# Kernel tuning notes

Measured on AMD Instinct MI355X. Metric: run time of the kernel, lower is better.

The kernel has to match this reference:

```python
import jax, jax.numpy as jnp
import numpy as np

N, M, D = 8192, 8192, 128
EPS = 1e-9


def setup_inputs() -> dict:
    key = jax.random.key(0)
    k1, k2 = jax.random.split(key)
    X = jax.random.normal(k1, (N, D), dtype=jnp.float32)
    Y = jax.random.normal(k2, (M, D), dtype=jnp.float32)
    sigma = jnp.ones((1,), dtype=jnp.float32)  # bandwidth (self.sigma)
    return {"X": X, "Y": Y, "sigma": sigma}


def reference(X, Y, sigma):
    # l2norm: ||x_i - y_j||^2 = ||x_i||^2 - 2 x_i.y_j + ||y_j||^2
    # (original builds full XX/YY Gram matrices just for their diagonals;
    #  same math via row-wise sums of squares)
    x2 = jnp.sum(X * X, axis=1)          # [n]
    y2 = jnp.sum(Y * Y, axis=1)          # [m]
    xy = jnp.matmul(X, Y.T)              # [n, m]
    dnorm2 = x2[:, None] - 2.0 * xy + y2[None, :]
    sigma2_inv = 1.0 / (sigma[0] ** 2 + EPS)
    K_XY = jnp.exp(-sigma2_inv * dnorm2)  # [n, m]
    return K_XY
```

## Files before the change

kernel.cpp:

```cpp
#include <hip/hip_runtime.h>
#include <stdint.h>

#define D_DIM 128
#define NROW 8192
#define MROW 8192
#define TILE 128
#define LDK2 72
#define OUT_LD 8192

typedef __bf16 bf16x8 __attribute__((ext_vector_type(8)));
typedef float f32x4 __attribute__((ext_vector_type(4)));

__device__ __forceinline__ unsigned short f32_to_bf16(float f) {
    uint32_t u = __float_as_uint(f);
    u = (u + 0x7FFFu + ((u >> 16) & 1u)) >> 16;
    return (unsigned short)u;
}

__global__ __launch_bounds__(256) void rbf_norms(const float* __restrict__ X,
                                                 const float* __restrict__ Y,
                                                 float* __restrict__ nrm) {
    const int t = threadIdx.x;
    const int w = t >> 6, lane = t & 63;
    const int rid = blockIdx.x * 4 + w;
    const float* src = (rid < NROW) ? (X + (size_t)rid * D_DIM)
                                    : (Y + (size_t)(rid - NROW) * D_DIM);
    float2 v = *(const float2*)(src + 2 * lane);
    float s = v.x * v.x + v.y * v.y;
    #pragma unroll
    for (int off = 32; off > 0; off >>= 1) s += __shfl_xor(s, off, 64);
    if (lane == 0) nrm[rid] = s;
}

__global__ __launch_bounds__(256, 4) void rbf_main(const float* __restrict__ X,
                                                   const float* __restrict__ Y,
                                                   const float* __restrict__ sigma,
                                                   const float* __restrict__ nrm,
                                                   float* __restrict__ out) {
    __shared__ unsigned short Xs[TILE][LDK2];
    __shared__ unsigned short Ys[TILE][LDK2];
    __shared__ float x2s[TILE];
    __shared__ float y2s[TILE];

    const int t = threadIdx.x;
    const int row0 = blockIdx.y * TILE;
    const int col0 = blockIdx.x * TILE;

    if (t < 128) x2s[t] = nrm[row0 + t];
    else         y2s[t - 128] = nrm[NROW + col0 + (t - 128)];

    const int w = t >> 6, ln = t & 63;
    const int quad = ln >> 4, l16 = ln & 15;
    const int wr = (w >> 1) * 64;
    const int wc = (w & 1) * 64;

    f32x4 acc[4][4] = {};

    #pragma unroll
    for (int p = 0; p < 2; ++p) {
        #pragma unroll
        for (int i = 0; i < 8; ++i) {
            int f = t + 256 * i;
            int r = f >> 4;
            int c = (f & 15) * 4;
            float4 vx = *(const float4*)(X + (size_t)(row0 + r) * D_DIM + p * 64 + c);
            float4 vy = *(const float4*)(Y + (size_t)(col0 + r) * D_DIM + p * 64 + c);
            ushort4 hx = { f32_to_bf16(vx.x), f32_to_bf16(vx.y), f32_to_bf16(vx.z), f32_to_bf16(vx.w) };
            ushort4 hy = { f32_to_bf16(vy.x), f32_to_bf16(vy.y), f32_to_bf16(vy.z), f32_to_bf16(vy.w) };
            *(ushort4*)(&Xs[r][c]) = hx;
            *(ushort4*)(&Ys[r][c]) = hy;
        }
        __syncthreads();

        #pragma unroll
        for (int ks = 0; ks < 2; ++ks) {
            const int k = ks * 32 + quad * 8;
            bf16x8 ax[4], by[4];
            #pragma unroll
            for (int ti = 0; ti < 4; ++ti)
                ax[ti] = *(const bf16x8*)(&Xs[wr + ti * 16 + l16][k]);
            #pragma unroll
            for (int tj = 0; tj < 4; ++tj)
                by[tj] = *(const bf16x8*)(&Ys[wc + tj * 16 + l16][k]);
            #pragma unroll
            for (int ti = 0; ti < 4; ++ti)
                #pragma unroll
                for (int tj = 0; tj < 4; ++tj)
                    acc[ti][tj] = __builtin_amdgcn_mfma_f32_16x16x32_bf16(by[tj], ax[ti], acc[ti][tj], 0, 0, 0);
        }
        if (p == 0) __syncthreads();
    }

    const float s2 = sigma[0] * sigma[0] + 1e-9f;
    const float cexp = -1.4426950408889634f / s2;

    float x2r[4];
    #pragma unroll
    for (int ti = 0; ti < 4; ++ti) x2r[ti] = x2s[wr + ti * 16 + l16];

    #pragma unroll
    for (int tj = 0; tj < 4; ++tj) {
        f32x4 y2v = *(const f32x4*)(&y2s[wc + tj * 16 + quad * 4]);
        size_t gcol = (size_t)(col0 + wc + tj * 16 + quad * 4);
        #pragma unroll
        for (int ti = 0; ti < 4; ++ti) {
            f32x4 v;
            #pragma unroll
            for (int r = 0; r < 4; ++r) {
                float d = x2r[ti] + y2v[r] - 2.0f * acc[ti][tj][r];
                v[r] = __builtin_amdgcn_exp2f(d * cexp);
            }
            size_t grow = (size_t)(row0 + wr + ti * 16 + l16);
            __builtin_nontemporal_store(v, (f32x4*)(out + grow * OUT_LD + gcol));
        }
    }
}

extern "C" void kernel_launch(void* const* d_in, const int* in_sizes, int n_in,
                              void* d_out, int out_size, void* d_ws, size_t ws_size,
                              hipStream_t stream) {
    const float* X = (const float*)d_in[0];
    const float* Y = (const float*)d_in[1];
    const float* sigma = (const float*)d_in[2];
    float* nrm = (float*)d_ws;
    float* out = (float*)d_out;

    rbf_norms<<<(NROW + MROW) / 4, 256, 0, stream>>>(X, Y, nrm);
    rbf_main<<<dim3(MROW / TILE, NROW / TILE), 256, 0, stream>>>(X, Y, sigma, nrm, out);
}
```

Before: 309.2 us.

## Load MFMA operands directly from global memory, removing LDS staging and barriers

Removes the shared-memory tiles and __syncthreads. Each wave now loads its X/Y fragments straight from global memory into registers and converts them to bf16 with native casts. Row norms are read directly from the workspace instead of through LDS. This drops the LDS round trips and the barriers. In exchange, each X/Y element is fetched by two waves instead of once per block, which relies on L1/L2 to absorb the duplicated traffic, and the global loads are less coalesced.

```diff
diff --git a/kernel.cpp b/kernel.cpp
--- a/kernel.cpp
+++ b/kernel.cpp
@@ -5,16 +5,16 @@
 #define NROW 8192
 #define MROW 8192
 #define TILE 128
-#define LDK2 72
 #define OUT_LD 8192
 
 typedef __bf16 bf16x8 __attribute__((ext_vector_type(8)));
 typedef float f32x4 __attribute__((ext_vector_type(4)));
 
-__device__ __forceinline__ unsigned short f32_to_bf16(float f) {
-    uint32_t u = __float_as_uint(f);
-    u = (u + 0x7FFFu + ((u >> 16) & 1u)) >> 16;
-    return (unsigned short)u;
+__device__ __forceinline__ bf16x8 cvt8(float4 u, float4 v) {
+    bf16x8 r;
+    r[0] = (__bf16)u.x; r[1] = (__bf16)u.y; r[2] = (__bf16)u.z; r[3] = (__bf16)u.w;
+    r[4] = (__bf16)v.x; r[5] = (__bf16)v.y; r[6] = (__bf16)v.z; r[7] = (__bf16)v.w;
+    return r;
 }
 
 __global__ __launch_bounds__(256) void rbf_norms(const float* __restrict__ X,
@@ -37,58 +37,34 @@
                                                    const float* __restrict__ sigma,
                                                    const float* __restrict__ nrm,
                                                    float* __restrict__ out) {
-    __shared__ unsigned short Xs[TILE][LDK2];
-    __shared__ unsigned short Ys[TILE][LDK2];
-    __shared__ float x2s[TILE];
-    __shared__ float y2s[TILE];
-
     const int t = threadIdx.x;
-    const int row0 = blockIdx.y * TILE;
-    const int col0 = blockIdx.x * TILE;
-
-    if (t < 128) x2s[t] = nrm[row0 + t];
-    else         y2s[t - 128] = nrm[NROW + col0 + (t - 128)];
-
     const int w = t >> 6, ln = t & 63;
     const int quad = ln >> 4, l16 = ln & 15;
-    const int wr = (w >> 1) * 64;
-    const int wc = (w & 1) * 64;
+    const int rw = blockIdx.y * TILE + (w >> 1) * 64;
+    const int cw = blockIdx.x * TILE + (w & 1) * 64;
+
+    const float* xr = X + (size_t)(rw + l16) * D_DIM + quad * 8;
+    const float* yr = Y + (size_t)(cw + l16) * D_DIM + quad * 8;
 
     f32x4 acc[4][4] = {};
-
     #pragma unroll
-    for (int p = 0; p < 2; ++p) {
+    for (int ks = 0; ks < 4; ++ks) {
+        bf16x8 a[4], b[4];
         #pragma unroll
-        for (int i = 0; i < 8; ++i) {
-            int f = t + 256 * i;
-            int r = f >> 4;
-            int c = (f & 15) * 4;
-            float4 vx = *(const float4*)(X + (size_t)(row0 + r) * D_DIM + p * 64 + c);
-            float4 vy = *(const float4*)(Y + (size_t)(col0 + r) * D_DIM + p * 64 + c);
-            ushort4 hx = { f32_to_bf16(vx.x), f32_to_bf16(vx.y), f32_to_bf16(vx.z), f32_to_bf16(vx.w) };
-            ushort4 hy = { f32_to_bf16(vy.x), f32_to_bf16(vy.y), f32_to_bf16(vy.z), f32_to_bf16(vy.w) };
-            *(ushort4*)(&Xs[r][c]) = hx;
-            *(ushort4*)(&Ys[r][c]) = hy;
+        for (int tj = 0; tj < 4; ++tj) {
+            const float* p = yr + tj * (16 * D_DIM) + ks * 32;
+            a[tj] = cvt8(*(const float4*)p, *(const float4*)(p + 4));
         }
-        __syncthreads();
-
         #pragma unroll
-        for (int ks = 0; ks < 2; ++ks) {
-            const int k = ks * 32 + quad * 8;
-            bf16x8 ax[4], by[4];
-            #pragma unroll
-            for (int ti = 0; ti < 4; ++ti)
-                ax[ti] = *(const bf16x8*)(&Xs[wr + ti * 16 + l16][k]);
+        for (int ti = 0; ti < 4; ++ti) {
+            const float* p = xr + ti * (16 * D_DIM) + ks * 32;
+            b[ti] = cvt8(*(const float4*)p, *(const float4*)(p + 4));
+        }
+        #pragma unroll
+        for (int ti = 0; ti < 4; ++ti)
             #pragma unroll
             for (int tj = 0; tj < 4; ++tj)
-                by[tj] = *(const bf16x8*)(&Ys[wc + tj * 16 + l16][k]);
-            #pragma unroll
-            for (int ti = 0; ti < 4; ++ti)
-                #pragma unroll
-                for (int tj = 0; tj < 4; ++tj)
-                    acc[ti][tj] = __builtin_amdgcn_mfma_f32_16x16x32_bf16(by[tj], ax[ti], acc[ti][tj], 0, 0, 0);
-        }
-        if (p == 0) __syncthreads();
+                acc[ti][tj] = __builtin_amdgcn_mfma_f32_16x16x32_bf16(a[tj], b[ti], acc[ti][tj], 0, 0, 0);
     }
 
     const float s2 = sigma[0] * sigma[0] + 1e-9f;
@@ -96,12 +72,12 @@
 
     float x2r[4];
     #pragma unroll
-    for (int ti = 0; ti < 4; ++ti) x2r[ti] = x2s[wr + ti * 16 + l16];
+    for (int ti = 0; ti < 4; ++ti) x2r[ti] = nrm[rw + ti * 16 + l16];
 
     #pragma unroll
     for (int tj = 0; tj < 4; ++tj) {
-        f32x4 y2v = *(const f32x4*)(&y2s[wc + tj * 16 + quad * 4]);
-        size_t gcol = (size_t)(col0 + wc + tj * 16 + quad * 4);
+        f32x4 y2v = *(const f32x4*)(nrm + NROW + cw + tj * 16 + quad * 4);
+        size_t gcol = (size_t)(cw + tj * 16 + quad * 4);
         #pragma unroll
         for (int ti = 0; ti < 4; ++ti) {
             f32x4 v;
@@ -110,7 +86,7 @@
                 float d = x2r[ti] + y2v[r] - 2.0f * acc[ti][tj][r];
                 v[r] = __builtin_amdgcn_exp2f(d * cexp);
             }
-            size_t grow = (size_t)(row0 + wr + ti * 16 + l16);
+            size_t grow = (size_t)(rw + ti * 16 + l16);
             __builtin_nontemporal_store(v, (f32x4*)(out + grow * OUT_LD + gcol));
         }
     }
```

New measurement: 379.3 us. 22.7% more time.

## Remap blocks per XCD for L2 locality, use native bf16 convert, drop norm LDS

Applied to the files above, without the earlier changes.

Flattens the grid to 1D and remaps block ids so that blocks landing on the same XCD (round-robin by id mod 8) cover a compact 8x8 group of output tiles, which raises L2 reuse of X and Y rows. It also replaces the manual round-to-nearest-even bf16 conversion with native casts, which may lower to hardware convert instructions. Norms are now read straight from global memory in the epilogue instead of being staged in shared memory. The kernel is dominated by writing the 256MB output, so the gains are limited to load traffic and instruction overhead.

```diff
diff --git a/kernel.cpp b/kernel.cpp
--- a/kernel.cpp
+++ b/kernel.cpp
@@ -11,10 +11,11 @@
 typedef __bf16 bf16x8 __attribute__((ext_vector_type(8)));
 typedef float f32x4 __attribute__((ext_vector_type(4)));
 
-__device__ __forceinline__ unsigned short f32_to_bf16(float f) {
-    uint32_t u = __float_as_uint(f);
-    u = (u + 0x7FFFu + ((u >> 16) & 1u)) >> 16;
-    return (unsigned short)u;
+__device__ __forceinline__ ushort4 cvt4(float4 v) {
+    union { __bf16 h[4]; ushort4 u; } r;
+    r.h[0] = (__bf16)v.x; r.h[1] = (__bf16)v.y;
+    r.h[2] = (__bf16)v.z; r.h[3] = (__bf16)v.w;
+    return r.u;
 }
 
 __global__ __launch_bounds__(256) void rbf_norms(const float* __restrict__ X,
@@ -39,16 +40,16 @@
                                                    float* __restrict__ out) {
     __shared__ unsigned short Xs[TILE][LDK2];
     __shared__ unsigned short Ys[TILE][LDK2];
-    __shared__ float x2s[TILE];
-    __shared__ float y2s[TILE];
+
+    const int b = blockIdx.x;
+    const int xcd = b & 7;
+    const int s = b >> 3;
+    const int grp = s >> 6;
+    const int i = s & 63;
+    const int row0 = (xcd * 8 + (i >> 3)) * TILE;
+    const int col0 = (grp * 8 + (i & 7)) * TILE;
 
     const int t = threadIdx.x;
-    const int row0 = blockIdx.y * TILE;
-    const int col0 = blockIdx.x * TILE;
-
-    if (t < 128) x2s[t] = nrm[row0 + t];
-    else         y2s[t - 128] = nrm[NROW + col0 + (t - 128)];
-
     const int w = t >> 6, ln = t & 63;
     const int quad = ln >> 4, l16 = ln & 15;
     const int wr = (w >> 1) * 64;
@@ -59,16 +60,14 @@
     #pragma unroll
     for (int p = 0; p < 2; ++p) {
         #pragma unroll
-        for (int i = 0; i < 8; ++i) {
-            int f = t + 256 * i;
+        for (int it = 0; it < 8; ++it) {
+            int f = t + 256 * it;
             int r = f >> 4;
             int c = (f & 15) * 4;
             float4 vx = *(const float4*)(X + (size_t)(row0 + r) * D_DIM + p * 64 + c);
             float4 vy = *(const float4*)(Y + (size_t)(col0 + r) * D_DIM + p * 64 + c);
-            ushort4 hx = { f32_to_bf16(vx.x), f32_to_bf16(vx.y), f32_to_bf16(vx.z), f32_to_bf16(vx.w) };
-            ushort4 hy = { f32_to_bf16(vy.x), f32_to_bf16(vy.y), f32_to_bf16(vy.z), f32_to_bf16(vy.w) };
-            *(ushort4*)(&Xs[r][c]) = hx;
-            *(ushort4*)(&Ys[r][c]) = hy;
+            *(ushort4*)(&Xs[r][c]) = cvt4(vx);
+            *(ushort4*)(&Ys[r][c]) = cvt4(vy);
         }
         __syncthreads();
 
@@ -94,23 +93,20 @@
     const float s2 = sigma[0] * sigma[0] + 1e-9f;
     const float cexp = -1.4426950408889634f / s2;
 
-    float x2r[4];
     #pragma unroll
-    for (int ti = 0; ti < 4; ++ti) x2r[ti] = x2s[wr + ti * 16 + l16];
-
-    #pragma unroll
-    for (int tj = 0; tj < 4; ++tj) {
-        f32x4 y2v = *(const f32x4*)(&y2s[wc + tj * 16 + quad * 4]);
-        size_t gcol = (size_t)(col0 + wc + tj * 16 + quad * 4);
+    for (int ti = 0; ti < 4; ++ti) {
+        const float x2 = nrm[row0 + wr + ti * 16 + l16];
+        const size_t grow = (size_t)(row0 + wr + ti * 16 + l16);
         #pragma unroll
-        for (int ti = 0; ti < 4; ++ti) {
+        for (int tj = 0; tj < 4; ++tj) {
+            f32x4 y2v = *(const f32x4*)(nrm + NROW + col0 + wc + tj * 16 + quad * 4);
             f32x4 v;
             #pragma unroll
             for (int r = 0; r < 4; ++r) {
-                float d = x2r[ti] + y2v[r] - 2.0f * acc[ti][tj][r];
+                float d = x2 + y2v[r] - 2.0f * acc[ti][tj][r];
                 v[r] = __builtin_amdgcn_exp2f(d * cexp);
             }
-            size_t grow = (size_t)(row0 + wr + ti * 16 + l16);
+            size_t gcol = (size_t)(col0 + wc + tj * 16 + quad * 4);
             __builtin_nontemporal_store(v, (f32x4*)(out + grow * OUT_LD + gcol));
         }
     }
@@ -126,5 +122,5 @@
     float* out = (float*)d_out;
 
     rbf_norms<<<(NROW + MROW) / 4, 256, 0, stream>>>(X, Y, nrm);
-    rbf_main<<<dim3(MROW / TILE, NROW / TILE), 256, 0, stream>>>(X, Y, sigma, nrm, out);
+    rbf_main<<<(NROW / TILE) * (MROW / TILE), 256, 0, stream>>>(X, Y, sigma, nrm, out);
 }
```

Measured after the change: 314.8 us. No clear change (+1.8%).
